# Optimization experiments

Measured on AMD Instinct MI355X. Metric: run time of the kernel, lower is better.

Reference implementation:

```python
import jax, jax.numpy as jnp
import numpy as np

QSP_DEPTH = 27  # -> 2*depth+1 = 55 phase parameters
B = 524288


def setup_inputs() -> dict:
    key = jax.random.key(0)
    k1, k2, k3 = jax.random.split(key, 3)
    x = jax.random.normal(k1, (B, 1), dtype=jnp.float32)
    qsp_params = jax.random.normal(k2, (2 * QSP_DEPTH + 1,), dtype=jnp.float32)
    alphas = jax.random.normal(k3, (B,), dtype=jnp.float32)
    bias = jnp.zeros((1,), dtype=jnp.float32)
    return {"x": x, "qsp_params": qsp_params, "alphas": alphas, "bias": bias}


def _qsp_expectation(theta, phis):
    """Quantum-signal-processing expectation Re(<0|U|0>) with
    U = S(phi_0) * prod_{k=1}^{2*depth} [ W(theta) S(phi_k) ],
    W(theta) = [[cos t, i sin t], [i sin t, cos t]] (X-rotation signal),
    S(phi) = diag(e^{i phi}, e^{-i phi}) (Z phase rotation).
    theta: (B,) float, phis: (2*depth+1,) float -> (B,) float.
    """
    c = jnp.cos(theta).astype(jnp.complex64)
    s = (1j * jnp.sin(theta).astype(jnp.complex64))
    # W: (B, 2, 2) signal rotation, shared across all chain steps
    W = jnp.stack([jnp.stack([c, s], axis=-1), jnp.stack([s, c], axis=-1)], axis=-2)

    P0 = jnp.broadcast_to(jnp.eye(2, dtype=jnp.complex64), W.shape)

    def step(P, phi):
        e = jnp.exp(1j * phi.astype(jnp.complex64))
        # right-multiply by diag(e, conj(e)) == column scaling of W
        M = W * jnp.stack([e, jnp.conj(e)])[None, None, :]
        return P @ M, None

    P, _ = jax.lax.scan(step, P0, phis[1:])  # 2*depth fixed-depth chain
    # left S(phi_0) only scales row 0 of <0|.|0> element
    amp00 = jnp.exp(1j * phis[0].astype(jnp.complex64)) * P[:, 0, 0]
    return jnp.real(amp00)


def reference(x, qsp_params, alphas, bias):
    theta = x[:, 0]                                   # (B,)
    qsp_val = _qsp_expectation(theta, qsp_params)     # (B,)
    preds = alphas * qsp_val + bias                   # (B,)
    return preds[:, None].astype(jnp.float32)         # (B, 1)
```

## Files before the change

kernel.cpp:

```cpp
#include <hip/hip_runtime.h>
#include <math.h>

constexpr int QSP_DEPTH = 27;
constexpr int NPHI  = 2 * QSP_DEPTH + 1;
constexpr int NSTEP = NPHI - 1;
constexpr int NDBL  = NSTEP / 2;
constexpr int MAXM  = NSTEP;
constexpr int NE    = 2 * MAXM + 1;
constexpr int NA    = NE + 4;
constexpr int NC    = MAXM / 2 + 1;
constexpr int NB    = 512;

__global__ __launch_bounds__(256) void qsp_fused_kernel(
    const float* __restrict__ x,
    const float* __restrict__ phis,
    const float* __restrict__ alphas,
    const float* __restrict__ bias,
    float* __restrict__ out, int n)
{
    __shared__ float2 U[2][NA], V[2][NA];
    __shared__ float cph[NSTEP], sph[NSTEP];
    __shared__ float cs[NC];

    const int t = threadIdx.x;

    if (t < NSTEP) {
        float s, c;
        sincosf(phis[t + 1], &s, &c);
        cph[t] = c; sph[t] = s;
    }
    if (t < NA) {
        U[0][t] = make_float2(0.f, 0.f); V[0][t] = make_float2(0.f, 0.f);
        U[1][t] = make_float2(0.f, 0.f); V[1][t] = make_float2(0.f, 0.f);
    }
    __syncthreads();
    if (t == 0) U[0][MAXM + 2] = make_float2(1.f, 0.f);
    __syncthreads();

    int src = 0;
    for (int s = 0; s < NDBL; ++s) {
        const int dst = src ^ 1;
        if (t < NE) {
            const int a = t + 2;
            const float2 um2 = U[src][a - 2], um0 = U[src][a], up2 = U[src][a + 2];
            const float2 vm2 = V[src][a - 2], vm0 = V[src][a], vp2 = V[src][a + 2];
            const float ca = cph[2 * s],     sa = sph[2 * s];
            const float cb = cph[2 * s + 1], sb = sph[2 * s + 1];

            float tr = 0.5f * (um2.x + um0.x + vm2.x - vm0.x);
            float ti = 0.5f * (um2.y + um0.y + vm2.y - vm0.y);
            const float uAm1r = ca * tr - sa * ti, uAm1i = ca * ti + sa * tr;
            tr = 0.5f * (um2.x - um0.x + vm2.x + vm0.x);
            ti = 0.5f * (um2.y - um0.y + vm2.y + vm0.y);
            const float vAm1r = ca * tr + sa * ti, vAm1i = ca * ti - sa * tr;
            tr = 0.5f * (um0.x + up2.x + vm0.x - vp2.x);
            ti = 0.5f * (um0.y + up2.y + vm0.y - vp2.y);
            const float uAp1r = ca * tr - sa * ti, uAp1i = ca * ti + sa * tr;
            tr = 0.5f * (um0.x - up2.x + vm0.x + vp2.x);
            ti = 0.5f * (um0.y - up2.y + vm0.y + vp2.y);
            const float vAp1r = ca * tr + sa * ti, vAp1i = ca * ti - sa * tr;

            tr = 0.5f * (uAm1r + uAp1r + vAm1r - vAp1r);
            ti = 0.5f * (uAm1i + uAp1i + vAm1i - vAp1i);
            U[dst][a] = make_float2(cb * tr - sb * ti, cb * ti + sb * tr);
            tr = 0.5f * (uAm1r - uAp1r + vAm1r + vAp1r);
            ti = 0.5f * (uAm1i - uAp1i + vAm1i + vAp1i);
            V[dst][a] = make_float2(cb * tr + sb * ti, cb * ti - sb * tr);
        }
        src ^= 1;
        __syncthreads();
    }

    if (t < NC) {
        float s0, c0;
        sincosf(phis[0], &s0, &c0);
        const float2 u = U[src][2 * t + MAXM + 2];
        const float re = c0 * u.x - s0 * u.y;
        cs[t] = (t ? 2.0f : 1.0f) * re;
    }
    __syncthreads();

    const float b0 = bias[0];
    const int nv = n >> 2;
    const float4* __restrict__ x4 = (const float4*)x;
    const float4* __restrict__ a4 = (const float4*)alphas;
    float4* __restrict__ o4 = (float4*)out;

    for (int i = blockIdx.x * blockDim.x + t; i < nv; i += NB * 256) {
        const float4 xv = x4[i];
        const float4 av = a4[i];
        float4 ov;
        float* xe = (float*)&xv; float* ae = (float*)&av; float* oe = (float*)&ov;
#pragma unroll
        for (int e = 0; e < 4; ++e) {
            const float y  = cosf(2.0f * xe[e]);
            const float y2 = 2.0f * y;
            float b1 = 0.0f, b2 = 0.0f;
#pragma unroll
            for (int l = NC - 1; l >= 1; --l) {
                const float bl = fmaf(y2, b1, cs[l] - b2);
                b2 = b1; b1 = bl;
            }
            oe[e] = fmaf(ae[e], fmaf(y, b1, cs[0] - b2), b0);
        }
        o4[i] = ov;
    }
}

extern "C" void kernel_launch(void* const* d_in, const int* in_sizes, int n_in,
                              void* d_out, int out_size, void* d_ws, size_t ws_size,
                              hipStream_t stream) {
    const float* x      = (const float*)d_in[0];
    const float* phis   = (const float*)d_in[1];
    const float* alphas = (const float*)d_in[2];
    const float* bias   = (const float*)d_in[3];
    float* out          = (float*)d_out;

    const int n = in_sizes[0];
    qsp_fused_kernel<<<NB, 256, 0, stream>>>(x, phis, alphas, bias, out, n);
}
```

Measured before the change: 71.43 us.

## Compute QSP Chebyshev coefficients in one wavefront with shuffles, prefetch inputs early

Replaces the shared-memory, barrier-per-step coefficient recurrence with a single-wavefront register recurrence that uses lane shuffles, so 27 block-wide barriers go away. Each thread now issues its x/alphas loads before the prologue to hide load latency. The grid-stride loop becomes one float4 per thread and cosf becomes the fast __cosf intrinsic. The launch still uses NB=512 blocks of 256 threads, which only covers 131072 float4s while nv is 131072 here, so coverage is exact for this size but larger n would be left unprocessed. __cosf also has lower accuracy for large arguments.

```diff
diff --git a/kernel.cpp b/kernel.cpp
--- a/kernel.cpp
+++ b/kernel.cpp
@@ -4,11 +4,7 @@
 constexpr int QSP_DEPTH = 27;
 constexpr int NPHI  = 2 * QSP_DEPTH + 1;
 constexpr int NSTEP = NPHI - 1;
-constexpr int NDBL  = NSTEP / 2;
-constexpr int MAXM  = NSTEP;
-constexpr int NE    = 2 * MAXM + 1;
-constexpr int NA    = NE + 4;
-constexpr int NC    = MAXM / 2 + 1;
+constexpr int NC    = NSTEP / 2 + 1;
 constexpr int NB    = 512;
 
 __global__ __launch_bounds__(256) void qsp_fused_kernel(
@@ -18,93 +14,74 @@
     const float* __restrict__ bias,
     float* __restrict__ out, int n)
 {
-    __shared__ float2 U[2][NA], V[2][NA];
     __shared__ float cph[NSTEP], sph[NSTEP];
     __shared__ float cs[NC];
 
     const int t = threadIdx.x;
+    const int i = blockIdx.x * 256 + t;
+    const int nv = n >> 2;
+    const bool live = (i < nv);
+
+    float4 xv = make_float4(0.f, 0.f, 0.f, 0.f);
+    float4 av = make_float4(0.f, 0.f, 0.f, 0.f);
+    if (live) {
+        xv = ((const float4*)x)[i];
+        av = ((const float4*)alphas)[i];
+    }
+    const float b0 = bias[0];
 
     if (t < NSTEP) {
         float s, c;
         sincosf(phis[t + 1], &s, &c);
         cph[t] = c; sph[t] = s;
     }
-    if (t < NA) {
-        U[0][t] = make_float2(0.f, 0.f); V[0][t] = make_float2(0.f, 0.f);
-        U[1][t] = make_float2(0.f, 0.f); V[1][t] = make_float2(0.f, 0.f);
-    }
-    __syncthreads();
-    if (t == 0) U[0][MAXM + 2] = make_float2(1.f, 0.f);
     __syncthreads();
 
-    int src = 0;
-    for (int s = 0; s < NDBL; ++s) {
-        const int dst = src ^ 1;
-        if (t < NE) {
-            const int a = t + 2;
-            const float2 um2 = U[src][a - 2], um0 = U[src][a], up2 = U[src][a + 2];
-            const float2 vm2 = V[src][a - 2], vm0 = V[src][a], vp2 = V[src][a + 2];
-            const float ca = cph[2 * s],     sa = sph[2 * s];
-            const float cb = cph[2 * s + 1], sb = sph[2 * s + 1];
-
-            float tr = 0.5f * (um2.x + um0.x + vm2.x - vm0.x);
-            float ti = 0.5f * (um2.y + um0.y + vm2.y - vm0.y);
-            const float uAm1r = ca * tr - sa * ti, uAm1i = ca * ti + sa * tr;
-            tr = 0.5f * (um2.x - um0.x + vm2.x + vm0.x);
-            ti = 0.5f * (um2.y - um0.y + vm2.y + vm0.y);
-            const float vAm1r = ca * tr + sa * ti, vAm1i = ca * ti - sa * tr;
-            tr = 0.5f * (um0.x + up2.x + vm0.x - vp2.x);
-            ti = 0.5f * (um0.y + up2.y + vm0.y - vp2.y);
-            const float uAp1r = ca * tr - sa * ti, uAp1i = ca * ti + sa * tr;
-            tr = 0.5f * (um0.x - up2.x + vm0.x + vp2.x);
-            ti = 0.5f * (um0.y - up2.y + vm0.y + vp2.y);
-            const float vAp1r = ca * tr + sa * ti, vAp1i = ca * ti - sa * tr;
-
-            tr = 0.5f * (uAm1r + uAp1r + vAm1r - vAp1r);
-            ti = 0.5f * (uAm1i + uAp1i + vAm1i - vAp1i);
-            U[dst][a] = make_float2(cb * tr - sb * ti, cb * ti + sb * tr);
-            tr = 0.5f * (uAm1r - uAp1r + vAm1r + vAp1r);
-            ti = 0.5f * (uAm1i - uAp1i + vAm1i + vAp1i);
-            V[dst][a] = make_float2(cb * tr + sb * ti, cb * ti - sb * tr);
+    if (t < 64) {
+        float uxr = (t == 0) ? 1.f : 0.f, uxi = 0.f;
+        float vxr = 0.f, vxi = 0.f;
+        for (int s = 0; s < NSTEP; ++s) {
+            const float c = cph[s], si = sph[s];
+            float umr = __shfl_up(uxr, 1);
+            float umi = __shfl_up(uxi, 1);
+            float vmr = __shfl_up(vxr, 1);
+            float vmi = __shfl_up(vxi, 1);
+            if (t == 0) { umr = 0.f; umi = 0.f; vmr = 0.f; vmi = 0.f; }
+            const float tur = 0.5f * (umr + uxr + vmr - vxr);
+            const float tui = 0.5f * (umi + uxi + vmi - vxi);
+            const float tvr = 0.5f * (umr - uxr + vmr + vxr);
+            const float tvi = 0.5f * (umi - uxi + vmi + vxi);
+            uxr = c * tur - si * tui;  uxi = c * tui + si * tur;
+            vxr = c * tvr + si * tvi;  vxi = c * tvi - si * tvr;
         }
-        src ^= 1;
-        __syncthreads();
-    }
-
-    if (t < NC) {
-        float s0, c0;
-        sincosf(phis[0], &s0, &c0);
-        const float2 u = U[src][2 * t + MAXM + 2];
-        const float re = c0 * u.x - s0 * u.y;
-        cs[t] = (t ? 2.0f : 1.0f) * re;
+        if (t >= 27 && t < 27 + NC) {
+            float s0, c0;
+            sincosf(phis[0], &s0, &c0);
+            const int l = t - 27;
+            cs[l] = (l ? 2.f : 1.f) * (c0 * uxr - s0 * uxi);
+        }
     }
     __syncthreads();
 
-    const float b0 = bias[0];
-    const int nv = n >> 2;
-    const float4* __restrict__ x4 = (const float4*)x;
-    const float4* __restrict__ a4 = (const float4*)alphas;
-    float4* __restrict__ o4 = (float4*)out;
+    if (!live) return;
 
-    for (int i = blockIdx.x * blockDim.x + t; i < nv; i += NB * 256) {
-        const float4 xv = x4[i];
-        const float4 av = a4[i];
-        float4 ov;
-        float* xe = (float*)&xv; float* ae = (float*)&av; float* oe = (float*)&ov;
+    float4 ov;
+    const float* xe = (const float*)&xv;
+    const float* ae = (const float*)&av;
+    float* oe = (float*)&ov;
 #pragma unroll
-        for (int e = 0; e < 4; ++e) {
-            const float y  = cosf(2.0f * xe[e]);
-            const float y2 = 2.0f * y;
-            float b1 = 0.0f, b2 = 0.0f;
+    for (int e = 0; e < 4; ++e) {
+        const float y  = __cosf(2.0f * xe[e]);
+        const float y2 = 2.0f * y;
+        float b1 = 0.f, b2 = 0.f;
 #pragma unroll
-            for (int l = NC - 1; l >= 1; --l) {
-                const float bl = fmaf(y2, b1, cs[l] - b2);
-                b2 = b1; b1 = bl;
-            }
-            oe[e] = fmaf(ae[e], fmaf(y, b1, cs[0] - b2), b0);
+        for (int l = NC - 1; l >= 1; --l) {
+            const float bl = fmaf(y2, b1, cs[l] - b2);
+            b2 = b1; b1 = bl;
         }
-        o4[i] = ov;
+        oe[e] = fmaf(ae[e], fmaf(y, b1, cs[0] - b2), b0);
     }
+    ((float4*)out)[i] = ov;
 }
 
 extern "C" void kernel_launch(void* const* d_in, const int* in_sizes, int n_in,
```

New measurement: 67.67 us. 1.06x faster.
